# Kernel optimization log

Measured on AMD Instinct MI355X. Metric: run time of the kernel, lower is better.

The kernel has to match this reference:

```python
import jax, jax.numpy as jnp
import numpy as np

# dims
B, L, H, NH, D = 512, 200, 128, 4, 32      # batch, seq_len, hidden, heads (gnn & fcb), head dim H/NH
FT, TP, IP = 32, 64, 200                    # first_taxonomy_num, taxonomy/item nodes per graph
NHOP, NB = 2, 2                             # n_hop gnn layers, gip_block_nums
SH, FH = 512, 256                           # scb_hidden_units, fcb_hidden_units
ITEMS, TAX = 100001, 2000                   # item vocab (+pad row 0), taxonomy vocab
NT, NI = B * TP, B * IP                     # total taxonomy / item nodes in batched forest
DEG_I, DEG_T = 4, 2                         # in-degree per taxonomy node for i2t / t2t edges


def _ln(x, g, b, eps=1e-8):
    m = jnp.mean(x, -1, keepdims=True)
    v = jnp.mean((x - m) ** 2, -1, keepdims=True)
    return (x - m) / jnp.sqrt(v + eps) * g + b


def _gat(src_h, dst_h, es, ed, W, al, ar, bias):
    """DGL GATConv (eval mode): shared fc, leaky_relu(0.2) scores, segment softmax,
    identity residual (in == heads*out), bias, ReLU activation."""
    fs = (src_h @ W).reshape(-1, NH, D)                 # [Ns,NH,D]
    fd = (dst_h @ W).reshape(-1, NH, D)                 # [Nd,NH,D]
    el = jnp.sum(fs * al, -1)                           # [Ns,NH]
    er = jnp.sum(fd * ar, -1)                           # [Nd,NH]
    e = jax.nn.leaky_relu(el[es] + er[ed], 0.2)         # [E,NH]
    emax = jax.ops.segment_max(e, ed, num_segments=NT)
    a = jnp.exp(e - emax[ed])
    s = jax.ops.segment_sum(a, ed, num_segments=NT)
    alpha = a / s[ed]                                   # [E,NH]
    rst = jax.ops.segment_sum(alpha[..., None] * fs[es], ed, num_segments=NT)
    rst = rst + dst_h.reshape(-1, NH, D) + bias.reshape(NH, D)
    return jax.nn.relu(rst).reshape(-1, NH * D)


def _forward(item_embed, tax_embed, scb_ln_g, scb_ln_b, scb_w1, scb_w2, fcb_ln_g, fcb_ln_b,
             fcb_w1, fcb_w2, fcb_w3, wv, gi_w, gi_al, gi_ar, gi_b, gt_w, gt_al, gt_ar, gt_b,
             liw_g, liw_b, int_g, int_b, uni_w,
             seq, root, i2t_src, i2t_dst, t2t_src, t2t_dst, item_ids, tax_ids):
    # --- global intention: mixer-style blocks over the item sequence ---
    V = item_embed[seq]                                           # [B,L,H]
    for i in range(NB):
        nv = _ln(V, scb_ln_g[i], scb_ln_b[i])
        t = jax.nn.gelu(jnp.einsum('blh,ls->bhs', nv, scb_w1[i]), approximate=False)
        vs = nv + jnp.einsum('bhs,sl->blh', t, scb_w2[i])         # seq-mixing block
        nvs = _ln(vs, fcb_ln_g[i], fcb_ln_b[i])
        xh = nvs.reshape(B, L, NH, D)                             # fcb heads share w1/w2
        y = jax.nn.gelu(jnp.einsum('blkc,cf->blkf', xh, fcb_w1[i]), approximate=False)
        y = jnp.einsum('blkf,fc->blkc', y, fcb_w2[i]).reshape(B, L, H)
        V = nvs + y @ fcb_w3[i]
    alpha = jax.nn.softmax(V @ wv, axis=1)                        # [B,L]
    g = jnp.sum(alpha[..., None] * V, axis=1)                     # [B,H]
    # --- local intention: multi-hop hetero GAT on batched item-taxonomy forest ---
    item_h = item_embed[item_ids]                                 # [NI,H]
    tax_h = tax_embed[tax_ids]                                    # [NT,H]
    acc = jnp.zeros_like(tax_h)
    for hop in range(NHOP):
        t_i = _gat(item_h, tax_h, i2t_src, i2t_dst, gi_w[hop], gi_al[hop], gi_ar[hop], gi_b[hop])
        t_t = _gat(tax_h, tax_h, t2t_src, t2t_dst, gt_w[hop], gt_al[hop], gt_ar[hop], gt_b[hop])
        tax_h = t_i + t_t                                         # HeteroGraphConv 'sum'
        acc = acc + tax_h                                         # k_list accumulation
    total = acc / NHOP                                            # average over hops
    offs = jnp.arange(B) * TP                                     # batched-graph offsets (graph_taxonomy)
    valid = root != -1
    local = jnp.where(valid[..., None], total[jnp.clip(root, 0) + offs[:, None]], 0.0)  # [B,FT,H]
    # --- fuse global + local ---
    mul = jnp.einsum('bfh,bh->bf', local, g)                      # [B,FT]
    w = jax.nn.softmax(jnp.where(mul != 0, _ln(mul, liw_g, liw_b), -jnp.inf), axis=-1)
    intention = _ln(g + jnp.sum(w[..., None] * local, axis=1), int_g, int_b)
    return (intention @ uni_w) @ item_embed.T                     # [B, ITEMS]


def setup_inputs():
    key = jax.random.key(0)
    ks = jax.random.split(key, 32)
    nrm = lambda i, sh: jax.random.normal(ks[i], sh, jnp.float32) * 0.05
    inp = {}
    inp['seq'] = jax.random.randint(ks[0], (B, L), 0, ITEMS)
    inp['root'] = jax.random.randint(ks[1], (B, FT), 0, TP)       # all valid roots
    i2t_dst = jnp.repeat(jnp.arange(NT), DEG_I)
    inp['i2t_dst'] = i2t_dst
    inp['i2t_src'] = (i2t_dst // TP) * IP + jax.random.randint(ks[2], (NT * DEG_I,), 0, IP)
    t2t_dst = jnp.repeat(jnp.arange(NT), DEG_T)
    inp['t2t_dst'] = t2t_dst
    inp['t2t_src'] = (t2t_dst // TP) * TP + jax.random.randint(ks[3], (NT * DEG_T,), 0, TP)
    inp['item_ids'] = jax.random.randint(ks[4], (NI,), 1, ITEMS)
    inp['tax_ids'] = jax.random.randint(ks[5], (NT,), 1, TAX)
    inp['item_embed'] = nrm(6, (ITEMS, H)).at[0].set(0.0)         # padding_idx=0
    inp['tax_embed'] = nrm(7, (TAX, H)).at[0].set(0.0)
    inp['scb_ln_g'] = jnp.ones((NB, H)); inp['scb_ln_b'] = jnp.zeros((NB, H))
    inp['scb_w1'] = nrm(8, (NB, L, SH)); inp['scb_w2'] = nrm(9, (NB, SH, L))
    inp['fcb_ln_g'] = jnp.ones((NB, H)); inp['fcb_ln_b'] = jnp.zeros((NB, H))
    inp['fcb_w1'] = nrm(10, (NB, D, FH)); inp['fcb_w2'] = nrm(11, (NB, FH, D))
    inp['fcb_w3'] = nrm(12, (NB, H, H))
    inp['wv'] = nrm(13, (H,))
    inp['gi_w'] = nrm(14, (NHOP, H, H)); inp['gi_al'] = nrm(15, (NHOP, NH, D))
    inp['gi_ar'] = nrm(16, (NHOP, NH, D)); inp['gi_b'] = nrm(17, (NHOP, H))
    inp['gt_w'] = nrm(18, (NHOP, H, H)); inp['gt_al'] = nrm(19, (NHOP, NH, D))
    inp['gt_ar'] = nrm(20, (NHOP, NH, D)); inp['gt_b'] = nrm(21, (NHOP, H))
    inp['liw_g'] = jnp.ones((FT,)); inp['liw_b'] = jnp.zeros((FT,))
    inp['int_g'] = jnp.ones((H,)); inp['int_b'] = jnp.zeros((H,))
    inp['uni_w'] = nrm(22, (H, H))
    return inp


def reference(item_embed, tax_embed, scb_ln_g, scb_ln_b, scb_w1, scb_w2, fcb_ln_g, fcb_ln_b,
              fcb_w1, fcb_w2, fcb_w3, wv, gi_w, gi_al, gi_ar, gi_b, gt_w, gt_al, gt_ar, gt_b,
              liw_g, liw_b, int_g, int_b, uni_w,
              seq, root, i2t_src, i2t_dst, t2t_src, t2t_dst, item_ids, tax_ids):
    return _forward(item_embed, tax_embed, scb_ln_g, scb_ln_b, scb_w1, scb_w2, fcb_ln_g, fcb_ln_b,
                    fcb_w1, fcb_w2, fcb_w3, wv, gi_w, gi_al, gi_ar, gi_b, gt_w, gt_al, gt_ar, gt_b,
                    liw_g, liw_b, int_g, int_b, uni_w,
                    seq, root, i2t_src, i2t_dst, t2t_src, t2t_dst, item_ids, tax_ids)
```

## Files before the change

### kernel.cpp

```cpp
#include <hip/hip_runtime.h>
#include <hip/hip_bf16.h>

constexpr int TB = 512, TL = 200, TH = 128, TNH = 4, TD = 32;
constexpr int TFT = 32, TTP = 64, TIP = 200;
constexpr int TSH = 512, TFH = 256;
constexpr int TITEMS = 100001;
constexpr int TNT = TB * TTP;
constexpr int TNI = TB * TIP;
constexpr int TLP = 224;
constexpr int TIPAD = 100096;

typedef __attribute__((ext_vector_type(8))) short short8v;
typedef __attribute__((ext_vector_type(4))) float f32x4;

__device__ inline float gelu_fast(float x) {
    float u = x + 0.044715f * x * x * x;
    float e = exp2f(-2.302208f * u);
    return x / (1.0f + e);
}
__device__ inline unsigned short to_bf16u(float x) {
    __hip_bfloat16 h = __float2bfloat16(x);
    return *reinterpret_cast<unsigned short*>(&h);
}
__device__ inline float bfu_to_f(unsigned short u) {
    unsigned int x = ((unsigned int)u) << 16;
    return __uint_as_float(x);
}

__device__ inline float block_reduce_sum(float v, float* red) {
    for (int o = 32; o > 0; o >>= 1) v += __shfl_down(v, o, 64);
    int nw = blockDim.x >> 6;
    if ((threadIdx.x & 63) == 0) red[threadIdx.x >> 6] = v;
    __syncthreads();
    float r = 0.f;
    for (int w = 0; w < nw; ++w) r += red[w];
    __syncthreads();
    return r;
}

__global__ __launch_bounds__(256) void k_gather_bf(const float* __restrict__ tab,
                                                   const int* __restrict__ idx,
                                                   unsigned short* __restrict__ out, int nrows) {
    int e = blockIdx.x * blockDim.x + threadIdx.x;
    if (e >= nrows * 16) return;
    int r = e >> 4, c = e & 15;
    const float4 a = ((const float4*)tab)[(size_t)idx[r] * 32 + c * 2];
    const float4 b = ((const float4*)tab)[(size_t)idx[r] * 32 + c * 2 + 1];
    uint4 u;
    u.x = (unsigned int)to_bf16u(a.x) | ((unsigned int)to_bf16u(a.y) << 16);
    u.y = (unsigned int)to_bf16u(a.z) | ((unsigned int)to_bf16u(a.w) << 16);
    u.z = (unsigned int)to_bf16u(b.x) | ((unsigned int)to_bf16u(b.y) << 16);
    u.w = (unsigned int)to_bf16u(b.z) | ((unsigned int)to_bf16u(b.w) << 16);
    *(uint4*)(out + (size_t)e * 8) = u;
}

__global__ __launch_bounds__(256) void k_wcvt(const float* __restrict__ fw1, const float* __restrict__ fw2,
                                              const float* __restrict__ fw3, const float* __restrict__ giw,
                                              const float* __restrict__ gtw, unsigned short* __restrict__ WB) {
    int idx = blockIdx.x * 256 + threadIdx.x;
    float v;
    if (idx < 16384) {
        int nb = idx >> 13, r = idx & 8191, n = r >> 5, k = r & 31;
        v = fw1[(size_t)nb * 8192 + k * 256 + n];
    } else if (idx < 32768) {
        int t = idx - 16384;
        int nb = t >> 13, r = t & 8191, n = r >> 8, k = r & 255;
        v = fw2[(size_t)nb * 8192 + k * 32 + n];
    } else if (idx < 65536) {
        int t = idx - 32768;
        int nb = t >> 14, r = t & 16383, n = r >> 7, k = r & 127;
        v = fw3[(size_t)nb * 16384 + k * 128 + n];
    } else if (idx < 98304) {
        int t = idx - 65536;
        int hop = t >> 14, r = t & 16383, n = r >> 7, k = r & 127;
        v = giw[(size_t)hop * 16384 + k * 128 + n];
    } else {
        int t = idx - 98304;
        int hop = t >> 14, r = t & 16383, n = r >> 7, k = r & 127;
        v = gtw[(size_t)hop * 16384 + k * 128 + n];
    }
    WB[idx] = to_bf16u(v);
}

__global__ __launch_bounds__(128) void k_lnt(const float* __restrict__ V,
                                             const int* __restrict__ seqp, const float* __restrict__ tab,
                                             const float* __restrict__ g, const float* __restrict__ b,
                                             float* __restrict__ NV, unsigned short* __restrict__ NVT) {
    __shared__ float tl[64][129];
    __shared__ float mrow[64], irow[64];
    int bb = blockIdx.y, l0 = blockIdx.x * 64, tid = threadIdx.x;
    for (int i = tid; i < 2048; i += 128) {
        int r = i >> 5, c = i & 31;
        int l = l0 + r;
        float4 v = {0.f, 0.f, 0.f, 0.f};
        if (l < TL) {
            const float* src = seqp ? (tab + (size_t)seqp[bb * TL + l] * TH)
                                    : (V + ((size_t)bb * TL + l) * TH);
            v = *(const float4*)(src + c * 4);
        }
        tl[r][c * 4 + 0] = v.x; tl[r][c * 4 + 1] = v.y;
        tl[r][c * 4 + 2] = v.z; tl[r][c * 4 + 3] = v.w;
    }
    __syncthreads();
    {
        int row = tid >> 1, half = tid & 1;
        float s = 0.f, sq = 0.f;
        for (int k = 0; k < 64; ++k) {
            float v = tl[row][half * 64 + k];
            s += v; sq += v * v;
        }
        s += __shfl_xor(s, 1);
        sq += __shfl_xor(sq, 1);
        if (half == 0) {
            float mean = s * (1.f / 128.f);
            mrow[row] = mean;
            irow[row] = rsqrtf(sq * (1.f / 128.f) - mean * mean + 1e-8f);
        }
    }
    __syncthreads();
    for (int i = tid; i < 2048; i += 128) {
        int r = i >> 5, c = i & 31;
        int l = l0 + r;
        float4 o = {0.f, 0.f, 0.f, 0.f};
        if (l < TL) {
            float4 v = *(float4*)&tl[r][c * 4];
            float m = mrow[r], inv = irow[r];
            const float4 gg = ((const float4*)g)[c];
            const float4 bv = ((const float4*)b)[c];
            o.x = (v.x - m) * inv * gg.x + bv.x;
            o.y = (v.y - m) * inv * gg.y + bv.y;
            o.z = (v.z - m) * inv * gg.z + bv.z;
            o.w = (v.w - m) * inv * gg.w + bv.w;
            *(float4*)(NV + ((size_t)bb * TL + l) * TH + c * 4) = o;
        }
        *(float4*)&tl[r][c * 4] = o;
    }
    __syncthreads();
    int h = tid;
    int ng = (l0 + 64 > TLP) ? (TLP - l0) / 8 : 8;
    for (int lg = 0; lg < ng; ++lg) {
        uint4 u;
        unsigned int p[4];
#pragma unroll
        for (int q = 0; q < 4; ++q) {
            unsigned short ua = to_bf16u(tl[lg * 8 + q * 2 + 0][h]);
            unsigned short ub = to_bf16u(tl[lg * 8 + q * 2 + 1][h]);
            p[q] = (unsigned int)ua | ((unsigned int)ub << 16);
        }
        u.x = p[0]; u.y = p[1]; u.z = p[2]; u.w = p[3];
        *(uint4*)(NVT + ((size_t)bb * TH + h) * TLP + l0 + lg * 8) = u;
    }
}

__global__ __launch_bounds__(256) void k_wscb(const float* __restrict__ w1, const float* __restrict__ w2,
                                              unsigned short* __restrict__ W1T,
                                              unsigned short* __restrict__ W2T) {
    int bx = blockIdx.x;
    if (bx < TSH) {
        int s = bx, l = threadIdx.x;
        if (l < TLP) W1T[(size_t)s * TLP + l] = to_bf16u(l < TL ? w1[(size_t)l * TSH + s] : 0.f);
    } else {
        int l = bx - TSH;
        for (int it = 0; it < 2; ++it) {
            int s = it * 256 + threadIdx.x;
            W2T[(size_t)l * TSH + s] = to_bf16u(l < TL ? w2[(size_t)s * TL + l] : 0.f);
        }
    }
}

__global__ __launch_bounds__(256) void k_mm1(const unsigned short* __restrict__ NVT,
                                             const unsigned short* __restrict__ W1T,
                                             unsigned short* __restrict__ T, int bh) {
    __shared__ unsigned short As[128][40];
    __shared__ unsigned short Bs[128][40];
    int tid = threadIdx.x;
    int b_local = blockIdx.y, b = bh * 256 + b_local;
    int s0 = blockIdx.x * 128;
    int lane = tid & 63, wid = tid >> 6;
    int mw = wid >> 1, nw = wid & 1;
    f32x4 accT[4][4];
#pragma unroll
    for (int j = 0; j < 4; ++j)
#pragma unroll
        for (int i = 0; i < 4; ++i) accT[j][i] = (f32x4){0.f, 0.f, 0.f, 0.f};
    const unsigned short* Abase = NVT + (size_t)b * TH * TLP;
    const unsigned short* Bbase = W1T + (size_t)s0 * TLP;
    for (int kc = 0; kc < 7; ++kc) {
        __syncthreads();
        for (int i = tid; i < 512; i += 256) {
            int r = i >> 2, q = i & 3;
            *(uint4*)&As[r][q * 8] = *(const uint4*)(Abase + (size_t)r * TLP + kc * 32 + q * 8);
            *(uint4*)&Bs[r][q * 8] = *(const uint4*)(Bbase + (size_t)r * TLP + kc * 32 + q * 8);
        }
        __syncthreads();
        int ko = (lane >> 4) * 8;
        short8v af[4], bfr[4];
#pragma unroll
        for (int t = 0; t < 4; ++t) {
            af[t] = *(const short8v*)&As[mw * 64 + t * 16 + (lane & 15)][ko];
            bfr[t] = *(const short8v*)&Bs[nw * 64 + t * 16 + (lane & 15)][ko];
        }
#pragma unroll
        for (int j = 0; j < 4; ++j)
#pragma unroll
            for (int i = 0; i < 4; ++i)
                accT[j][i] = __builtin_amdgcn_mfma_f32_16x16x32_bf16(bfr[j], af[i], accT[j][i], 0, 0, 0);
    }
    int rbase = (lane >> 4) * 4, col = lane & 15;
#pragma unroll
    for (int i = 0; i < 4; ++i)
#pragma unroll
        for (int j = 0; j < 4; ++j) {
            int h = mw * 64 + i * 16 + col;
            int sb = s0 + nw * 64 + j * 16 + rbase;
            ushort4 pk;
            pk.x = to_bf16u(gelu_fast(accT[j][i][0]));
            pk.y = to_bf16u(gelu_fast(accT[j][i][1]));
            pk.z = to_bf16u(gelu_fast(accT[j][i][2]));
            pk.w = to_bf16u(gelu_fast(accT[j][i][3]));
            *(ushort4*)(T + ((size_t)b_local * TH + h) * TSH + sb) = pk;
        }
}

__global__ __launch_bounds__(256) void k_mm2l(const unsigned short* __restrict__ T,
                                              const unsigned short* __restrict__ W2T,
                                              float* __restrict__ NV,
                                              const float* __restrict__ lg, const float* __restrict__ lb,
                                              int bh) {
    __shared__ unsigned short As[128][40];
    __shared__ unsigned short Bs[64][40];
    __shared__ float vsl[64][132];
    __shared__ float mrow[64], irow[64];
    int tid = threadIdx.x;
    int b_local = blockIdx.y, b = bh * 256 + b_local;
    int l0 = blockIdx.x * 64;
    int lane = tid & 63, wid = tid >> 6;
    f32x4 acc[2][4];
#pragma unroll
    for (int i = 0; i < 2; ++i)
#pragma unroll
        for (int j = 0; j < 4; ++j) acc[i][j] = (f32x4){0.f, 0.f, 0.f, 0.f};
    const unsigned short* Abase = T + (size_t)b_local * TH * TSH;
    for (int kc = 0; kc < 16; ++kc) {
        __syncthreads();
        for (int i = tid; i < 512; i += 256) {
            int r = i >> 2, q = i & 3;
            *(uint4*)&As[r][q * 8] = *(const uint4*)(Abase + (size_t)r * TSH + kc * 32 + q * 8);
        }
        {
            int r = tid >> 2, q = tid & 3;
            int l = l0 + r;
            uint4 v = {0u, 0u, 0u, 0u};
            if (l < 208) v = *(const uint4*)(W2T + (size_t)l * TSH + kc * 32 + q * 8);
            *(uint4*)&Bs[r][q * 8] = v;
        }
        __syncthreads();
        int ko = (lane >> 4) * 8;
        short8v af[2], bfr[4];
#pragma unroll
        for (int t = 0; t < 2; ++t)
            af[t] = *(const short8v*)&As[wid * 32 + t * 16 + (lane & 15)][ko];
#pragma unroll
        for (int j = 0; j < 4; ++j)
            bfr[j] = *(const short8v*)&Bs[j * 16 + (lane & 15)][ko];
#pragma unroll
        for (int i = 0; i < 2; ++i)
#pragma unroll
            for (int j = 0; j < 4; ++j)
                acc[i][j] = __builtin_amdgcn_mfma_f32_16x16x32_bf16(af[i], bfr[j], acc[i][j], 0, 0, 0);
    }
    int rbase = (lane >> 4) * 4, col = lane & 15;
#pragma unroll
    for (int i = 0; i < 2; ++i)
#pragma unroll
        for (int j = 0; j < 4; ++j) {
            int l = l0 + j * 16 + col;
            int h0 = wid * 32 + i * 16 + rbase;
            float4 res = {0.f, 0.f, 0.f, 0.f};
            if (l < TL) res = *(const float4*)(NV + ((size_t)b * TL + l) * TH + h0);
            float4 o;
            o.x = acc[i][j][0] + res.x;
            o.y = acc[i][j][1] + res.y;
            o.z = acc[i][j][2] + res.z;
            o.w = acc[i][j][3] + res.w;
            *(float4*)&vsl[j * 16 + col][h0] = o;
        }
    __syncthreads();
    int row = tid >> 2, q = tid & 3;
    {
        float s = 0.f, sq = 0.f;
        for (int k = 0; k < 32; ++k) {
            float v = vsl[row][q * 32 + k];
            s += v; sq += v * v;
        }
        s += __shfl_xor(s, 1); s += __shfl_xor(s, 2);
        sq += __shfl_xor(sq, 1); sq += __shfl_xor(sq, 2);
        if (q == 0) {
            float mean = s * (1.f / 128.f);
            mrow[row] = mean;
            irow[row] = rsqrtf(sq * (1.f / 128.f) - mean * mean + 1e-8f);
        }
    }
    __syncthreads();
    {
        int l = l0 + row;
        if (l < TL) {
            float mean = mrow[row], inv = irow[row];
            float* dst = NV + ((size_t)b * TL + l) * TH + q * 32;
#pragma unroll
            for (int k4 = 0; k4 < 8; ++k4) {
                float4 v = *(float4*)&vsl[row][q * 32 + k4 * 4];
                const float4 gg = ((const float4*)lg)[q * 8 + k4];
                const float4 bv = ((const float4*)lb)[q * 8 + k4];
                float4 o;
                o.x = (v.x - mean) * inv * gg.x + bv.x;
                o.y = (v.y - mean) * inv * gg.y + bv.y;
                o.z = (v.z - mean) * inv * gg.z + bv.z;
                o.w = (v.w - mean) * inv * gg.w + bv.w;
                *(float4*)(dst + k4 * 4) = o;
            }
        }
    }
}

__global__ __launch_bounds__(256) void k_ffuse(const float* __restrict__ NV,
                                               const unsigned short* __restrict__ FW1B,
                                               const unsigned short* __restrict__ FW2B,
                                               unsigned short* __restrict__ Z, int ntiles) {
    __shared__ unsigned short As[64][40];
    __shared__ unsigned short Bs2[32 * 264];
    __shared__ unsigned short Yl[64 * 264];
    int tid = threadIdx.x;
    int lane = tid & 63, wid = tid >> 6;
    int col = lane & 15, rbase = (lane >> 4) * 4, ko = (lane >> 4) * 8;
    for (int i = tid; i < 1024; i += 256) {
        int r = i >> 2, q = i & 3;
        *(uint4*)&Yl[r * 40 + q * 8] = *(const uint4*)(FW1B + r * 32 + q * 8);
    }
    for (int i = tid; i < 1024; i += 256) {
        int r = i >> 5, q = i & 31;
        *(uint4*)&Bs2[r * 264 + q * 8] = *(const uint4*)(FW2B + r * 256 + q * 8);
    }
    __syncthreads();
    short8v bfr[4];
#pragma unroll
    for (int t = 0; t < 4; ++t)
        bfr[t] = *(const short8v*)&Yl[(wid * 64 + t * 16 + col) * 40 + ko];
    __syncthreads();
    int mrow = wid * 16 + col;
    int sw2 = ((mrow >> 2) & 7) << 3;
    for (int tile = blockIdx.x; tile < ntiles; tile += gridDim.x) {
        int m0 = tile * 64;
        for (int i = tid; i < 512; i += 256) {
            int r = i >> 3, q = i & 7;
            const float4 v = *(const float4*)(NV + (size_t)(m0 + r) * 32 + q * 4);
            ushort4 u;
            u.x = to_bf16u(v.x); u.y = to_bf16u(v.y); u.z = to_bf16u(v.z); u.w = to_bf16u(v.w);
            *(ushort4*)&As[r][q * 4] = u;
        }
        __syncthreads();
        {
            short8v af[4];
#pragma unroll
            for (int t = 0; t < 4; ++t)
                af[t] = *(const short8v*)&As[t * 16 + col][ko];
            f32x4 yt[4][4];
#pragma unroll
            for (int j = 0; j < 4; ++j)
#pragma unroll
                for (int i = 0; i < 4; ++i) yt[j][i] = (f32x4){0.f, 0.f, 0.f, 0.f};
#pragma unroll
            for (int j = 0; j < 4; ++j)
#pragma unroll
                for (int i = 0; i < 4; ++i)
                    yt[j][i] = __builtin_amdgcn_mfma_f32_16x16x32_bf16(bfr[j], af[i], yt[j][i], 0, 0, 0);
#pragma unroll
            for (int i = 0; i < 4; ++i)
#pragma unroll
                for (int j = 0; j < 4; ++j) {
                    int m = i * 16 + col;
                    int n0 = wid * 64 + j * 16 + rbase;
                    ushort4 pk;
                    pk.x = to_bf16u(gelu_fast(yt[j][i][0]));
                    pk.y = to_bf16u(gelu_fast(yt[j][i][1]));
                    pk.z = to_bf16u(gelu_fast(yt[j][i][2]));
                    pk.w = to_bf16u(gelu_fast(yt[j][i][3]));
                    int idx = (m * 264 + n0) ^ (((m >> 2) & 7) << 3);
                    *(ushort4*)&Yl[idx] = pk;
                }
        }
        __syncthreads();
        {
            f32x4 acc2[2];
            acc2[0] = (f32x4){0.f, 0.f, 0.f, 0.f};
            acc2[1] = (f32x4){0.f, 0.f, 0.f, 0.f};
            for (int kc = 0; kc < 8; ++kc) {
                int ko2 = kc * 32 + ko;
                short8v a2 = *(const short8v*)&Yl[(mrow * 264 + ko2) ^ sw2];
                short8v b0 = *(const short8v*)&Bs2[col * 264 + ko2];
                short8v b1 = *(const short8v*)&Bs2[(16 + col) * 264 + ko2];
                acc2[0] = __builtin_amdgcn_mfma_f32_16x16x32_bf16(a2, b0, acc2[0], 0, 0, 0);
                acc2[1] = __builtin_amdgcn_mfma_f32_16x16x32_bf16(a2, b1, acc2[1], 0, 0, 0);
            }
#pragma unroll
            for (int j = 0; j < 2; ++j)
#pragma unroll
                for (int r = 0; r < 4; ++r)
                    Z[(size_t)(m0 + wid * 16 + rbase + r) * 32 + j * 16 + col] =
                        to_bf16u(acc2[j][r]);
        }
        __syncthreads();
    }
}

__global__ __launch_bounds__(256) void k_gmm_b(const unsigned short* __restrict__ A,
                                               const unsigned short* __restrict__ WB,
                                               const float* __restrict__ R,
                                               float* __restrict__ C) {
    __shared__ unsigned short As[128][40];
    __shared__ unsigned short Bs[128][40];
    int tid = threadIdx.x;
    int m0 = blockIdx.x * 128;
    int lane = tid & 63, wid = tid >> 6;
    int mw = wid >> 1, nw = wid & 1;
    f32x4 acc[4][4];
#pragma unroll
    for (int i = 0; i < 4; ++i)
#pragma unroll
        for (int j = 0; j < 4; ++j) acc[i][j] = (f32x4){0.f, 0.f, 0.f, 0.f};
    for (int kc = 0; kc < 4; ++kc) {
        __syncthreads();
        for (int i = tid; i < 512; i += 256) {
            int r = i >> 2, q = i & 3;
            *(uint4*)&As[r][q * 8] = *(const uint4*)(A + (size_t)(m0 + r) * TH + kc * 32 + q * 8);
            *(uint4*)&Bs[r][q * 8] = *(const uint4*)(WB + (size_t)r * TH + kc * 32 + q * 8);
        }
        __syncthreads();
        int ko = (lane >> 4) * 8;
        short8v af[4], bfr[4];
#pragma unroll
        for (int t = 0; t < 4; ++t) {
            af[t] = *(const short8v*)&As[mw * 64 + t * 16 + (lane & 15)][ko];
            bfr[t] = *(const short8v*)&Bs[nw * 64 + t * 16 + (lane & 15)][ko];
        }
#pragma unroll
        for (int i = 0; i < 4; ++i)
#pragma unroll
            for (int j = 0; j < 4; ++j)
                acc[i][j] = __builtin_amdgcn_mfma_f32_16x16x32_bf16(af[i], bfr[j], acc[i][j], 0, 0, 0);
    }
    int rbase = (lane >> 4) * 4, col = lane & 15;
#pragma unroll
    for (int i = 0; i < 4; ++i)
#pragma unroll
        for (int j = 0; j < 4; ++j) {
            int n = nw * 64 + j * 16 + col;
#pragma unroll
            for (int r = 0; r < 4; ++r) {
                size_t off = (size_t)(m0 + mw * 64 + i * 16 + rbase + r) * TH + n;
                float v = acc[i][j][r];
                if (R) v += R[off];
                C[off] = v;
            }
        }
}

__global__ __launch_bounds__(256) void k_gmm3(
        const unsigned short* __restrict__ A0, const unsigned short* __restrict__ W0,
        unsigned short* __restrict__ C0, int nb0,
        const unsigned short* __restrict__ A1, const unsigned short* __restrict__ W1,
        unsigned short* __restrict__ C1, int nb1,
        const unsigned short* __restrict__ A2, const unsigned short* __restrict__ W2,
        unsigned short* __restrict__ C2) {
    __shared__ unsigned short As[128][40];
    __shared__ unsigned short Bs[128][40];
    int bx = blockIdx.x;
    const unsigned short *A, *WBp;
    unsigned short* C;
    if (bx < nb0) { A = A0; WBp = W0; C = C0; }
    else if (bx - nb0 < nb1) { bx -= nb0; A = A1; WBp = W1; C = C1; }
    else { bx -= nb0 + nb1; A = A2; WBp = W2; C = C2; }
    int tid = threadIdx.x;
    int m0 = bx * 128;
    int lane = tid & 63, wid = tid >> 6;
    int mw = wid >> 1, nw = wid & 1;
    f32x4 accT[4][4];
#pragma unroll
    for (int j = 0; j < 4; ++j)
#pragma unroll
        for (int i = 0; i < 4; ++i) accT[j][i] = (f32x4){0.f, 0.f, 0.f, 0.f};
    for (int kc = 0; kc < 4; ++kc) {
        __syncthreads();
        for (int i = tid; i < 512; i += 256) {
            int r = i >> 2, q = i & 3;
            *(uint4*)&As[r][q * 8] = *(const uint4*)(A + (size_t)(m0 + r) * TH + kc * 32 + q * 8);
            *(uint4*)&Bs[r][q * 8] = *(const uint4*)(WBp + (size_t)r * TH + kc * 32 + q * 8);
        }
        __syncthreads();
        int ko = (lane >> 4) * 8;
        short8v af[4], bfr[4];
#pragma unroll
        for (int t = 0; t < 4; ++t) {
            af[t] = *(const short8v*)&As[mw * 64 + t * 16 + (lane & 15)][ko];
            bfr[t] = *(const short8v*)&Bs[nw * 64 + t * 16 + (lane & 15)][ko];
        }
#pragma unroll
        for (int j = 0; j < 4; ++j)
#pragma unroll
            for (int i = 0; i < 4; ++i)
                accT[j][i] = __builtin_amdgcn_mfma_f32_16x16x32_bf16(bfr[j], af[i], accT[j][i], 0, 0, 0);
    }
    int rbase = (lane >> 4) * 4, col = lane & 15;
#pragma unroll
    for (int i = 0; i < 4; ++i)
#pragma unroll
        for (int j = 0; j < 4; ++j) {
            int m = m0 + mw * 64 + i * 16 + col;
            int n0 = nw * 64 + j * 16 + rbase;
            ushort4 pk;
            pk.x = to_bf16u(accT[j][i][0]);
            pk.y = to_bf16u(accT[j][i][1]);
            pk.z = to_bf16u(accT[j][i][2]);
            pk.w = to_bf16u(accT[j][i][3]);
            *(ushort4*)(C + (size_t)m * TH + n0) = pk;
        }
}

__global__ __launch_bounds__(256) void k_pool(const float* __restrict__ V, const float* __restrict__ wv,
                                              float* __restrict__ g) {
    __shared__ float sc[TL];
    __shared__ float red[4];
    int b = blockIdx.x, tid = threadIdx.x;
    int lane = tid & 63, w = tid >> 6;
    for (int l = w; l < TL; l += 4) {
        const float2 v = ((const float2*)(V + (size_t)(b * TL + l) * TH))[lane];
        float a = v.x * wv[2 * lane] + v.y * wv[2 * lane + 1];
        for (int o = 32; o > 0; o >>= 1) a += __shfl_down(a, o, 64);
        if (lane == 0) sc[l] = a;
    }
    __syncthreads();
    float m = (tid < TL) ? sc[tid] : -INFINITY;
    for (int o = 32; o > 0; o >>= 1) m = fmaxf(m, __shfl_down(m, o, 64));
    if ((tid & 63) == 0) red[tid >> 6] = m;
    __syncthreads();
    m = fmaxf(fmaxf(red[0], red[1]), fmaxf(red[2], red[3]));
    __syncthreads();
    float e = (tid < TL) ? expf(sc[tid] - m) : 0.f;
    float s = block_reduce_sum(e, red);
    if (tid < TL) sc[tid] = e / s;
    __syncthreads();
    if (tid < TH) {
        float a = 0.f;
        for (int l = 0; l < TL; ++l) a += sc[l] * V[(size_t)(b * TL + l) * TH + tid];
        g[b * TH + tid] = a;
    }
}

__global__ __launch_bounds__(256) void k_scores4(
        const unsigned short* __restrict__ f0, const float* __restrict__ v0, float* __restrict__ o0, int n0,
        const unsigned short* __restrict__ f1, const float* __restrict__ v1, float* __restrict__ o1, int n1,
        const unsigned short* __restrict__ f2, const float* __restrict__ v2, float* __restrict__ o2, int n2,
        const unsigned short* __restrict__ f3, const float* __restrict__ v3, float* __restrict__ o3, int n3) {
    int t = blockIdx.x * 256 + threadIdx.x;
    const unsigned short* f; const float* vec; float* o;
    if (t < n0 * 4) { f = f0; vec = v0; o = o0; }
    else {
        t -= n0 * 4;
        if (t < n1 * 4) { f = f1; vec = v1; o = o1; }
        else {
            t -= n1 * 4;
            if (t < n2 * 4) { f = f2; vec = v2; o = o2; }
            else {
                t -= n2 * 4;
                if (t >= n3 * 4) return;
                f = f3; vec = v3; o = o3;
            }
        }
    }
    int node = t >> 2, k = t & 3;
    const unsigned short* fp = f + (size_t)node * TH + k * TD;
    const float* vp = vec + k * TD;
    float a = 0.f;
#pragma unroll
    for (int q = 0; q < 4; ++q) {
        uint4 u = *(const uint4*)(fp + q * 8);
        unsigned int ws[4] = {u.x, u.y, u.z, u.w};
#pragma unroll
        for (int p = 0; p < 4; ++p) {
            a += __uint_as_float(ws[p] << 16) * vp[q * 8 + p * 2];
            a += __uint_as_float(ws[p] & 0xffff0000u) * vp[q * 8 + p * 2 + 1];
        }
    }
    o[t] = a;
}

__global__ __launch_bounds__(128) void k_gat(const unsigned short* __restrict__ tax_cur,
                                             const unsigned short* __restrict__ fs_i, const float* __restrict__ el_i,
                                             const float* __restrict__ er_i, const int* __restrict__ src_i,
                                             const float* __restrict__ bi,
                                             const unsigned short* __restrict__ fs_t, const float* __restrict__ el_t,
                                             const float* __restrict__ er_t, const int* __restrict__ src_t,
                                             const float* __restrict__ bt,
                                             unsigned short* __restrict__ tax_nxt,
                                             float* __restrict__ acc, int hop) {
    int n = blockIdx.x, h = threadIdx.x, k = h >> 5;
    float cur = bfu_to_f(tax_cur[(size_t)n * TH + h]);
    float ti, tt2;
    {
        float er = er_i[n * 4 + k];
        int s[4]; float e[4]; float m = -INFINITY;
#pragma unroll
        for (int j = 0; j < 4; ++j) {
            s[j] = src_i[n * 4 + j];
            float xx = el_i[s[j] * 4 + k] + er;
            e[j] = xx > 0.f ? xx : 0.2f * xx;
            m = fmaxf(m, e[j]);
        }
        float ssum = 0.f, av = 0.f;
#pragma unroll
        for (int j = 0; j < 4; ++j) {
            float a = expf(e[j] - m);
            ssum += a;
            av += a * bfu_to_f(fs_i[(size_t)s[j] * TH + h]);
        }
        ti = fmaxf(av / ssum + cur + bi[h], 0.f);
    }
    {
        float er = er_t[n * 4 + k];
        int s[2]; float e[2]; float m = -INFINITY;
#pragma unroll
        for (int j = 0; j < 2; ++j) {
            s[j] = src_t[n * 2 + j];
            float xx = el_t[s[j] * 4 + k] + er;
            e[j] = xx > 0.f ? xx : 0.2f * xx;
            m = fmaxf(m, e[j]);
        }
        float ssum = 0.f, av = 0.f;
#pragma unroll
        for (int j = 0; j < 2; ++j) {
            float a = expf(e[j] - m);
            ssum += a;
            av += a * bfu_to_f(fs_t[(size_t)s[j] * TH + h]);
        }
        tt2 = fmaxf(av / ssum + cur + bt[h], 0.f);
    }
    float nx = ti + tt2;
    size_t ai = (size_t)n * TH + h;
    tax_nxt[ai] = to_bf16u(nx);
    acc[ai] = (hop == 0) ? nx : acc[ai] + nx;
}

__global__ __launch_bounds__(128) void k_locfuse(const int* __restrict__ root, const float* __restrict__ acc,
                                                 const float* __restrict__ g,
                                                 const float* __restrict__ liw_g, const float* __restrict__ liw_b,
                                                 const float* __restrict__ int_g, const float* __restrict__ int_b,
                                                 const float* __restrict__ uni_w,
                                                 unsigned short* __restrict__ PB) {
    __shared__ float loc[TFT][TH];
    __shared__ float lm[TFT], wv_[TFT], inten[TH];
    __shared__ float red[2];
    int b = blockIdx.x, tid = threadIdx.x;
    float gv = g[b * TH + tid];
    for (int f = 0; f < TFT; ++f) {
        int r = root[b * TFT + f];
        float v = 0.f;
        if (r != -1) v = acc[(size_t)(b * TTP + (r < 0 ? 0 : r)) * TH + tid] * 0.5f;
        loc[f][tid] = v;
        float s = block_reduce_sum(v * gv, red);
        if (tid == 0) lm[f] = s;
    }
    __syncthreads();
    if (tid < TFT) {
        float mean = 0.f;
        for (int f = 0; f < TFT; ++f) mean += lm[f];
        mean *= (1.f / TFT);
        float var = 0.f;
        for (int f = 0; f < TFT; ++f) { float d = lm[f] - mean; var += d * d; }
        var *= (1.f / TFT);
        float ln = (lm[tid] - mean) * rsqrtf(var + 1e-8f) * liw_g[tid] + liw_b[tid];
        wv_[tid] = (lm[tid] != 0.f) ? ln : -INFINITY;
    }
    __syncthreads();
    if (tid < TFT) {
        float mx = -INFINITY;
        for (int f = 0; f < TFT; ++f) mx = fmaxf(mx, wv_[f]);
        float s = 0.f;
        for (int f = 0; f < TFT; ++f) s += expf(wv_[f] - mx);
        lm[tid] = expf(wv_[tid] - mx) / s;
    }
    __syncthreads();
    float ip = gv;
    for (int f = 0; f < TFT; ++f) ip += lm[f] * loc[f][tid];
    float mean = block_reduce_sum(ip, red) * (1.f / TH);
    float d = ip - mean;
    float var = block_reduce_sum(d * d, red) * (1.f / TH);
    inten[tid] = d * rsqrtf(var + 1e-8f) * int_g[tid] + int_b[tid];
    __syncthreads();
    float a = 0.f;
    for (int hp = 0; hp < TH; ++hp) a += inten[hp] * uni_w[hp * TH + tid];
    PB[(size_t)b * TH + tid] = to_bf16u(a);
}

__global__ __launch_bounds__(256) void k_final_m2(const unsigned short* __restrict__ PB,
                                                  const float* __restrict__ E,
                                                  float* __restrict__ out) {
    __shared__ unsigned short Bs[128][136];
    int tid = threadIdx.x;
    int i0 = blockIdx.x * 128;
    for (int i = tid; i < 2048; i += 256) {
        int r = i >> 4, q = i & 15;
        int it = i0 + r;
        float4 a = {0.f, 0.f, 0.f, 0.f}, b = {0.f, 0.f, 0.f, 0.f};
        if (it < TITEMS) {
            a = *(const float4*)(E + (size_t)it * TH + q * 8);
            b = *(const float4*)(E + (size_t)it * TH + q * 8 + 4);
        }
        ushort4 u0, u1;
        u0.x = to_bf16u(a.x); u0.y = to_bf16u(a.y); u0.z = to_bf16u(a.z); u0.w = to_bf16u(a.w);
        u1.x = to_bf16u(b.x); u1.y = to_bf16u(b.y); u1.z = to_bf16u(b.z); u1.w = to_bf16u(b.w);
        *(ushort4*)&Bs[r][q * 8] = u0;
        *(ushort4*)&Bs[r][q * 8 + 4] = u1;
    }
    __syncthreads();
    int lane = tid & 63, wid = tid >> 6;
    int mw = wid >> 1, nw = wid & 1;
    int rbase = (lane >> 4) * 4, col = lane & 15;
#pragma unroll 1
    for (int b0 = 0; b0 < TB; b0 += 128) {
        f32x4 acc[4][4];
#pragma unroll
        for (int i = 0; i < 4; ++i)
#pragma unroll
            for (int j = 0; j < 4; ++j) acc[i][j] = (f32x4){0.f, 0.f, 0.f, 0.f};
#pragma unroll
        for (int kc = 0; kc < 4; ++kc) {
            int ko = kc * 32 + (lane >> 4) * 8;
            short8v af[4], bfr[4];
#pragma unroll
            for (int t = 0; t < 4; ++t) {
                af[t] = *(const short8v*)(PB + (size_t)(b0 + mw * 64 + t * 16 + (lane & 15)) * TH + ko);
                bfr[t] = *(const short8v*)&Bs[nw * 64 + t * 16 + (lane & 15)][ko];
            }
#pragma unroll
            for (int i = 0; i < 4; ++i)
#pragma unroll
                for (int j = 0; j < 4; ++j)
                    acc[i][j] = __builtin_amdgcn_mfma_f32_16x16x32_bf16(af[i], bfr[j], acc[i][j], 0, 0, 0);
        }
#pragma unroll
        for (int i = 0; i < 4; ++i)
#pragma unroll
            for (int j = 0; j < 4; ++j) {
                int ii = i0 + nw * 64 + j * 16 + col;
                if (ii < TITEMS) {
#pragma unroll
                    for (int r = 0; r < 4; ++r)
                        out[(size_t)(b0 + mw * 64 + i * 16 + rbase + r) * TITEMS + ii] = acc[i][j][r];
                }
            }
    }
}

extern "C" void kernel_launch(void* const* d_in, const int* in_sizes, int n_in,
                              void* d_out, int out_size, void* d_ws, size_t ws_size,
                              hipStream_t stream) {
    const int*   seq        = (const int*)d_in[0];
    const int*   root       = (const int*)d_in[1];
    const int*   i2t_src    = (const int*)d_in[3];
    const int*   t2t_src    = (const int*)d_in[5];
    const int*   item_ids   = (const int*)d_in[6];
    const int*   tax_ids    = (const int*)d_in[7];
    const float* item_embed = (const float*)d_in[8];
    const float* tax_embed  = (const float*)d_in[9];
    const float* scb_ln_g   = (const float*)d_in[10];
    const float* scb_ln_b   = (const float*)d_in[11];
    const float* scb_w1     = (const float*)d_in[12];
    const float* scb_w2     = (const float*)d_in[13];
    const float* fcb_ln_g   = (const float*)d_in[14];
    const float* fcb_ln_b   = (const float*)d_in[15];
    const float* fcb_w1     = (const float*)d_in[16];
    const float* fcb_w2     = (const float*)d_in[17];
    const float* fcb_w3     = (const float*)d_in[18];
    const float* wv         = (const float*)d_in[19];
    const float* gi_w       = (const float*)d_in[20];
    const float* gi_al      = (const float*)d_in[21];
    const float* gi_ar      = (const float*)d_in[22];
    const float* gi_b       = (const float*)d_in[23];
    const float* gt_w       = (const float*)d_in[24];
    const float* gt_al      = (const float*)d_in[25];
    const float* gt_ar      = (const float*)d_in[26];
    const float* gt_b       = (const float*)d_in[27];
    const float* liw_g      = (const float*)d_in[28];
    const float* liw_b      = (const float*)d_in[29];
    const float* int_g      = (const float*)d_in[30];
    const float* int_b      = (const float*)d_in[31];
    const float* uni_w      = (const float*)d_in[32];

    char* w = (char*)d_ws;
    float* V     = (float*)(w + 0);
    float* NV    = (float*)(w + 52428800);
    unsigned short* FSIB   = (unsigned short*)(w + 0);
    unsigned short* ITEMHB = (unsigned short*)(w + 52428800);
    unsigned short* NVT = (unsigned short*)(w + 104857600);
    unsigned short* T   = (unsigned short*)(w + 134217728);
    unsigned short* W1T = (unsigned short*)(w + 167772160);
    unsigned short* W2T = (unsigned short*)(w + 168001536);
    unsigned short* ZB  = (unsigned short*)(w + 104857600);
    unsigned short* TAXB0 = (unsigned short*)(w + 104857600);
    unsigned short* TAXB1 = (unsigned short*)(w + 113246208);
    float* ACC   = (float*)(w + 138412032);
    unsigned short* FDIB = (unsigned short*)(w + 155189248);
    unsigned short* FSTB = (unsigned short*)(w + 171966464);
    float* ELI   = (float*)(w + 188743680);
    float* ERI   = (float*)(w + 190382080);
    float* ELT   = (float*)(w + 190906368);
    float* ERT   = (float*)(w + 191430656);
    float* G     = (float*)(w + 200343552);
    unsigned short* WB = (unsigned short*)(w + 191954944);
    unsigned short* PB = (unsigned short*)(w + 200671232);
    if (ws_size < 200933376ull) return;

    k_wcvt<<<512, 256, 0, stream>>>(fcb_w1, fcb_w2, fcb_w3, gi_w, gt_w, WB);

    for (int nb = 0; nb < 2; ++nb) {
        k_lnt<<<dim3(4, TB), 128, 0, stream>>>(V, nb == 0 ? seq : nullptr, item_embed,
                                               scb_ln_g + nb * TH, scb_ln_b + nb * TH, NV, NVT);
        k_wscb<<<720, 256, 0, stream>>>(scb_w1 + nb * TL * TSH, scb_w2 + nb * TSH * TL, W1T, W2T);
        for (int bh = 0; bh < 2; ++bh) {
            k_mm1<<<dim3(4, 256), 256, 0, stream>>>(NVT, W1T, T, bh);
            k_mm2l<<<dim3(4, 256), 256, 0, stream>>>(T, W2T, NV,
                                                     fcb_ln_g + nb * TH, fcb_ln_b + nb * TH, bh);
        }
        k_ffuse<<<1024, 256, 0, stream>>>(NV, WB + nb * 8192, WB + 16384 + nb * 8192, ZB,
                                          TB * TL * 4 / 64);
        k_gmm_b<<<TB * TL / 128, 256, 0, stream>>>(ZB, WB + 32768 + nb * 16384, NV, V);
    }
    k_pool<<<TB, 256, 0, stream>>>(V, wv, G);

    k_gather_bf<<<(TNI * 16 + 255) / 256, 256, 0, stream>>>(item_embed, item_ids, ITEMHB, TNI);
    k_gather_bf<<<(TNT * 16 + 255) / 256, 256, 0, stream>>>(tax_embed, tax_ids, TAXB0, TNT);

    unsigned short* curb = TAXB0;
    unsigned short* nxtb = TAXB1;
    for (int hop = 0; hop < 2; ++hop) {
        const unsigned short* WiB = WB + 65536 + hop * 16384;
        const unsigned short* WtB = WB + 98304 + hop * 16384;
        k_gmm3<<<TNI / 128 + 2 * (TNT / 128), 256, 0, stream>>>(
            ITEMHB, WiB, FSIB, TNI / 128,
            curb, WiB, FDIB, TNT / 128,
            curb, WtB, FSTB);
        int total = (TNI + 3 * TNT) * TNH;
        k_scores4<<<(total + 255) / 256, 256, 0, stream>>>(
            FSIB, gi_al + hop * TH, ELI, TNI,
            FDIB, gi_ar + hop * TH, ERI, TNT,
            FSTB, gt_al + hop * TH, ELT, TNT,
            FSTB, gt_ar + hop * TH, ERT, TNT);
        k_gat<<<TNT, 128, 0, stream>>>(curb, FSIB, ELI, ERI, i2t_src, gi_b + hop * TH,
                                       FSTB, ELT, ERT, t2t_src, gt_b + hop * TH, nxtb, ACC, hop);
        unsigned short* tmp = curb; curb = nxtb; nxtb = tmp;
    }

    k_locfuse<<<TB, 128, 0, stream>>>(root, ACC, G, liw_g, liw_b, int_g, int_b, uni_w, PB);
    k_final_m2<<<TIPAD / 128, 256, 0, stream>>>(PB, item_embed, (float*)d_out);
}
```

Baseline: 1.002 ms.

## Merge launches, hoist SCB weight conversion, compact workspace, parallelize pool and LM dot

Converts both SCB blocks' weights in one kernel before the loop and runs mm1/mm2l over the full batch in single launches instead of two halves. The two embedding gathers are merged into one launch. The workspace is reorganized so V aliases NV, with k_gmm_b writing its result in place, which shrinks the footprint so the full-batch T buffer fits. k_pool splits the weighted sum across all 256 threads, and the local-intention kernel replaces 32 serial block reductions with a padded shared-memory dot product. The aim is fewer launches, less serialization and better thread utilization, at the risk of aliasing mistakes from the in-place NV update.

```diff
diff --git a/kernel.cpp b/kernel.cpp
--- a/kernel.cpp
+++ b/kernel.cpp
@@ -38,11 +38,20 @@
     return r;
 }
 
-__global__ __launch_bounds__(256) void k_gather_bf(const float* __restrict__ tab,
-                                                   const int* __restrict__ idx,
-                                                   unsigned short* __restrict__ out, int nrows) {
-    int e = blockIdx.x * blockDim.x + threadIdx.x;
-    if (e >= nrows * 16) return;
+__global__ __launch_bounds__(256) void k_gather2(const float* __restrict__ tab0,
+                                                 const int* __restrict__ idx0,
+                                                 unsigned short* __restrict__ out0, int n0,
+                                                 const float* __restrict__ tab1,
+                                                 const int* __restrict__ idx1,
+                                                 unsigned short* __restrict__ out1, int n1) {
+    int e = blockIdx.x * 256 + threadIdx.x;
+    const float* tab; const int* idx; unsigned short* out;
+    if (e < n0 * 16) { tab = tab0; idx = idx0; out = out0; }
+    else {
+        e -= n0 * 16;
+        if (e >= n1 * 16) return;
+        tab = tab1; idx = idx1; out = out1;
+    }
     int r = e >> 4, c = e & 15;
     const float4 a = ((const float4*)tab)[(size_t)idx[r] * 32 + c * 2];
     const float4 b = ((const float4*)tab)[(size_t)idx[r] * 32 + c * 2 + 1];
@@ -82,6 +91,26 @@
     WB[idx] = to_bf16u(v);
 }
 
+__global__ __launch_bounds__(256) void k_wscb2(const float* __restrict__ w1, const float* __restrict__ w2,
+                                               unsigned short* __restrict__ W1T,
+                                               unsigned short* __restrict__ W2T) {
+    int bx = blockIdx.x;
+    if (bx < 1024) {
+        int nb = bx >> 9, s = bx & 511, l = threadIdx.x;
+        if (l < TLP)
+            W1T[(size_t)nb * 114688 + (size_t)s * TLP + l] =
+                to_bf16u(l < TL ? w1[(size_t)nb * 102400 + l * TSH + s] : 0.f);
+    } else {
+        int t = bx - 1024;
+        int nb = t / 208, l = t % 208;
+        for (int it = 0; it < 2; ++it) {
+            int s = it * 256 + threadIdx.x;
+            W2T[(size_t)nb * 106496 + (size_t)l * TSH + s] =
+                to_bf16u(l < TL ? w2[(size_t)nb * 102400 + s * TL + l] : 0.f);
+        }
+    }
+}
+
 __global__ __launch_bounds__(128) void k_lnt(const float* __restrict__ V,
                                              const int* __restrict__ seqp, const float* __restrict__ tab,
                                              const float* __restrict__ g, const float* __restrict__ b,
@@ -152,29 +181,13 @@
     }
 }
 
-__global__ __launch_bounds__(256) void k_wscb(const float* __restrict__ w1, const float* __restrict__ w2,
-                                              unsigned short* __restrict__ W1T,
-                                              unsigned short* __restrict__ W2T) {
-    int bx = blockIdx.x;
-    if (bx < TSH) {
-        int s = bx, l = threadIdx.x;
-        if (l < TLP) W1T[(size_t)s * TLP + l] = to_bf16u(l < TL ? w1[(size_t)l * TSH + s] : 0.f);
-    } else {
-        int l = bx - TSH;
-        for (int it = 0; it < 2; ++it) {
-            int s = it * 256 + threadIdx.x;
-            W2T[(size_t)l * TSH + s] = to_bf16u(l < TL ? w2[(size_t)s * TL + l] : 0.f);
-        }
-    }
-}
-
 __global__ __launch_bounds__(256) void k_mm1(const unsigned short* __restrict__ NVT,
                                              const unsigned short* __restrict__ W1T,
-                                             unsigned short* __restrict__ T, int bh) {
+                                             unsigned short* __restrict__ T) {
     __shared__ unsigned short As[128][40];
     __shared__ unsigned short Bs[128][40];
     int tid = threadIdx.x;
-    int b_local = blockIdx.y, b = bh * 256 + b_local;
+    int b = blockIdx.y;
     int s0 = blockIdx.x * 128;
     int lane = tid & 63, wid = tid >> 6;
     int mw = wid >> 1, nw = wid & 1;
@@ -218,21 +231,20 @@
             pk.y = to_bf16u(gelu_fast(accT[j][i][1]));
             pk.z = to_bf16u(gelu_fast(accT[j][i][2]));
             pk.w = to_bf16u(gelu_fast(accT[j][i][3]));
-            *(ushort4*)(T + ((size_t)b_local * TH + h) * TSH + sb) = pk;
+            *(ushort4*)(T + ((size_t)b * TH + h) * TSH + sb) = pk;
         }
 }
 
 __global__ __launch_bounds__(256) void k_mm2l(const unsigned short* __restrict__ T,
                                               const unsigned short* __restrict__ W2T,
                                               float* __restrict__ NV,
-                                              const float* __restrict__ lg, const float* __restrict__ lb,
-                                              int bh) {
+                                              const float* __restrict__ lg, const float* __restrict__ lb) {
     __shared__ unsigned short As[128][40];
     __shared__ unsigned short Bs[64][40];
     __shared__ float vsl[64][132];
     __shared__ float mrow[64], irow[64];
     int tid = threadIdx.x;
-    int b_local = blockIdx.y, b = bh * 256 + b_local;
+    int b = blockIdx.y;
     int l0 = blockIdx.x * 64;
     int lane = tid & 63, wid = tid >> 6;
     f32x4 acc[2][4];
@@ -240,7 +252,7 @@
     for (int i = 0; i < 2; ++i)
 #pragma unroll
         for (int j = 0; j < 4; ++j) acc[i][j] = (f32x4){0.f, 0.f, 0.f, 0.f};
-    const unsigned short* Abase = T + (size_t)b_local * TH * TSH;
+    const unsigned short* Abase = T + (size_t)b * TH * TSH;
     for (int kc = 0; kc < 16; ++kc) {
         __syncthreads();
         for (int i = tid; i < 512; i += 256) {
@@ -530,6 +542,7 @@
                                               float* __restrict__ g) {
     __shared__ float sc[TL];
     __shared__ float red[4];
+    __shared__ float part[TH];
     int b = blockIdx.x, tid = threadIdx.x;
     int lane = tid & 63, w = tid >> 6;
     for (int l = w; l < TL; l += 4) {
@@ -549,10 +562,14 @@
     float s = block_reduce_sum(e, red);
     if (tid < TL) sc[tid] = e / s;
     __syncthreads();
-    if (tid < TH) {
+    {
+        int h = tid & 127, half = tid >> 7;
         float a = 0.f;
-        for (int l = 0; l < TL; ++l) a += sc[l] * V[(size_t)(b * TL + l) * TH + tid];
-        g[b * TH + tid] = a;
+        for (int l = half * 100; l < half * 100 + 100; ++l)
+            a += sc[l] * V[(size_t)(b * TL + l) * TH + h];
+        if (half) part[h] = a;
+        __syncthreads();
+        if (!half) g[b * TH + h] = a + part[h];
     }
 }
 
@@ -656,18 +673,29 @@
                                                  const float* __restrict__ int_g, const float* __restrict__ int_b,
                                                  const float* __restrict__ uni_w,
                                                  unsigned short* __restrict__ PB) {
-    __shared__ float loc[TFT][TH];
+    __shared__ float loc[TFT][TH + 1];
+    __shared__ float gsh[TH];
     __shared__ float lm[TFT], wv_[TFT], inten[TH];
     __shared__ float red[2];
     int b = blockIdx.x, tid = threadIdx.x;
     float gv = g[b * TH + tid];
+    gsh[tid] = gv;
     for (int f = 0; f < TFT; ++f) {
         int r = root[b * TFT + f];
         float v = 0.f;
         if (r != -1) v = acc[(size_t)(b * TTP + (r < 0 ? 0 : r)) * TH + tid] * 0.5f;
         loc[f][tid] = v;
-        float s = block_reduce_sum(v * gv, red);
-        if (tid == 0) lm[f] = s;
+    }
+    __syncthreads();
+    {
+        int f = tid >> 2, q = tid & 3;
+        float a = 0.f;
+        const float* lp = &loc[f][q * 32];
+        const float* gp = &gsh[q * 32];
+        for (int k = 0; k < 32; ++k) a += lp[k] * gp[k];
+        a += __shfl_xor(a, 1);
+        a += __shfl_xor(a, 2);
+        if (q == 0) lm[f] = a;
     }
     __syncthreads();
     if (tid < TFT) {
@@ -797,48 +825,45 @@
     const float* uni_w      = (const float*)d_in[32];
 
     char* w = (char*)d_ws;
-    float* V     = (float*)(w + 0);
-    float* NV    = (float*)(w + 52428800);
-    unsigned short* FSIB   = (unsigned short*)(w + 0);
-    unsigned short* ITEMHB = (unsigned short*)(w + 52428800);
-    unsigned short* NVT = (unsigned short*)(w + 104857600);
-    unsigned short* T   = (unsigned short*)(w + 134217728);
-    unsigned short* W1T = (unsigned short*)(w + 167772160);
-    unsigned short* W2T = (unsigned short*)(w + 168001536);
-    unsigned short* ZB  = (unsigned short*)(w + 104857600);
-    unsigned short* TAXB0 = (unsigned short*)(w + 104857600);
-    unsigned short* TAXB1 = (unsigned short*)(w + 113246208);
-    float* ACC   = (float*)(w + 138412032);
-    unsigned short* FDIB = (unsigned short*)(w + 155189248);
-    unsigned short* FSTB = (unsigned short*)(w + 171966464);
-    float* ELI   = (float*)(w + 188743680);
-    float* ERI   = (float*)(w + 190382080);
-    float* ELT   = (float*)(w + 190906368);
-    float* ERT   = (float*)(w + 191430656);
+    float* NV  = (float*)(w + 0);
+    unsigned short* NVT = (unsigned short*)(w + 52428800);
+    unsigned short* ZB  = NVT;
+    unsigned short* T   = (unsigned short*)(w + 81788928);
+    unsigned short* W1T2 = (unsigned short*)(w + 148897792);
+    unsigned short* W2T2 = (unsigned short*)(w + 149356544);
+    unsigned short* ITEMHB = (unsigned short*)(w + 0);
+    unsigned short* FSIB   = (unsigned short*)(w + 26214400);
+    unsigned short* TAXB0  = (unsigned short*)(w + 52428800);
+    unsigned short* TAXB1  = (unsigned short*)(w + 60817408);
+    float* ACC   = (float*)(w + 69206016);
+    unsigned short* FDIB = (unsigned short*)(w + 85983232);
+    unsigned short* FSTB = (unsigned short*)(w + 94371840);
+    float* ELI   = (float*)(w + 102760448);
+    float* ERI   = (float*)(w + 104398848);
+    float* ELT   = (float*)(w + 104923136);
+    float* ERT   = (float*)(w + 105447424);
+    unsigned short* WB = (unsigned short*)(w + 191954944);
     float* G     = (float*)(w + 200343552);
-    unsigned short* WB = (unsigned short*)(w + 191954944);
     unsigned short* PB = (unsigned short*)(w + 200671232);
     if (ws_size < 200933376ull) return;
 
     k_wcvt<<<512, 256, 0, stream>>>(fcb_w1, fcb_w2, fcb_w3, gi_w, gt_w, WB);
+    k_wscb2<<<1440, 256, 0, stream>>>(scb_w1, scb_w2, W1T2, W2T2);
 
     for (int nb = 0; nb < 2; ++nb) {
-        k_lnt<<<dim3(4, TB), 128, 0, stream>>>(V, nb == 0 ? seq : nullptr, item_embed,
+        k_lnt<<<dim3(4, TB), 128, 0, stream>>>(NV, nb == 0 ? seq : nullptr, item_embed,
                                                scb_ln_g + nb * TH, scb_ln_b + nb * TH, NV, NVT);
-        k_wscb<<<720, 256, 0, stream>>>(scb_w1 + nb * TL * TSH, scb_w2 + nb * TSH * TL, W1T, W2T);
-        for (int bh = 0; bh < 2; ++bh) {
-            k_mm1<<<dim3(4, 256), 256, 0, stream>>>(NVT, W1T, T, bh);
-            k_mm2l<<<dim3(4, 256), 256, 0, stream>>>(T, W2T, NV,
-                                                     fcb_ln_g + nb * TH, fcb_ln_b + nb * TH, bh);
-        }
+        k_mm1<<<dim3(4, TB), 256, 0, stream>>>(NVT, W1T2 + nb * 114688, T);
+        k_mm2l<<<dim3(4, TB), 256, 0, stream>>>(T, W2T2 + nb * 106496, NV,
+                                                fcb_ln_g + nb * TH, fcb_ln_b + nb * TH);
         k_ffuse<<<1024, 256, 0, stream>>>(NV, WB + nb * 8192, WB + 16384 + nb * 8192, ZB,
                                           TB * TL * 4 / 64);
-        k_gmm_b<<<TB * TL / 128, 256, 0, stream>>>(ZB, WB + 32768 + nb * 16384, NV, V);
-    }
-    k_pool<<<TB, 256, 0, stream>>>(V, wv, G);
-
-    k_gather_bf<<<(TNI * 16 + 255) / 256, 256, 0, stream>>>(item_embed, item_ids, ITEMHB, TNI);
-    k_gather_bf<<<(TNT * 16 + 255) / 256, 256, 0, stream>>>(tax_embed, tax_ids, TAXB0, TNT);
+        k_gmm_b<<<TB * TL / 128, 256, 0, stream>>>(ZB, WB + 32768 + nb * 16384, NV, NV);
+    }
+    k_pool<<<TB, 256, 0, stream>>>(NV, wv, G);
+
+    k_gather2<<<(TNI * 16 + TNT * 16 + 255) / 256, 256, 0, stream>>>(
+        item_embed, item_ids, ITEMHB, TNI, tax_embed, tax_ids, TAXB0, TNT);
 
     unsigned short* curb = TAXB0;
     unsigned short* nxtb = TAXB1;
```

Result: faster. 951.0 us (-5.1%).
